# Kernel optimization log

Hardware: AMD Instinct MI355X
Metric: run time of the kernel (lower is better)

The kernel has to match this reference:

```python
import jax, jax.numpy as jnp
import numpy as np

N_NODES = 50000
N_EDGES = 800000
D_IN = 128
D_HID = 128
N_CLASSES = 40


def setup_inputs() -> dict:
    key = jax.random.key(0)
    ks = jax.random.split(key, 12)
    x = jax.random.normal(ks[0], (N_NODES, D_IN), dtype=jnp.float32)
    edge_index = jax.random.randint(ks[1], (2, N_EDGES), 0, N_NODES, dtype=jnp.int64)
    s1 = 1.0 / np.sqrt(D_IN)
    s2 = 1.0 / np.sqrt(D_HID)
    W1 = jax.random.uniform(ks[2], (D_IN, D_HID), jnp.float32, -s1, s1)
    b1 = jnp.zeros((D_HID,), jnp.float32)
    W2 = jax.random.uniform(ks[3], (D_HID, D_HID), jnp.float32, -s2, s2)
    b2 = jnp.zeros((D_HID,), jnp.float32)
    W3 = jax.random.uniform(ks[4], (D_HID, D_HID), jnp.float32, -s2, s2)
    b3 = jnp.zeros((D_HID,), jnp.float32)
    fcW = jax.random.uniform(ks[5], (D_HID, N_CLASSES), jnp.float32, -s2, s2)
    fcb = jax.random.uniform(ks[6], (N_CLASSES,), jnp.float32, -s2, s2)
    return {"x": x, "edge_index": edge_index, "W1": W1, "b1": b1,
            "W2": W2, "b2": b2, "W3": W3, "b3": b3, "fcW": fcW, "fcb": fcb}


def _gcn_norm(edge_index, n_nodes):
    # add self-loops, compute symmetric normalization deg^-1/2[src]*deg^-1/2[dst]
    loops = jnp.arange(n_nodes, dtype=edge_index.dtype)
    src = jnp.concatenate([edge_index[0], loops])
    dst = jnp.concatenate([edge_index[1], loops])
    deg = jax.ops.segment_sum(jnp.ones_like(dst, dtype=jnp.float32), dst,
                              num_segments=n_nodes)
    dinv = jax.lax.rsqrt(deg)  # deg >= 1 thanks to self-loops
    norm = dinv[src] * dinv[dst]  # [E+N]
    return src, dst, norm


def _gcn_conv(h, W, b, src, dst, norm, n_nodes):
    h = h @ W                               # [N, D]
    msg = h[src] * norm[:, None]            # [E+N, D] gather + scale
    out = jax.ops.segment_sum(msg, dst, num_segments=n_nodes)  # scatter-add
    return out + b


def reference(x, edge_index, W1, b1, W2, b2, W3, b3, fcW, fcb):
    n = x.shape[0]
    src, dst, norm = _gcn_norm(edge_index, n)
    h = jax.nn.relu(_gcn_conv(x, W1, b1, src, dst, norm, n))
    h = jax.nn.relu(_gcn_conv(h, W2, b2, src, dst, norm, n))
    h = jax.nn.relu(_gcn_conv(h, W3, b3, src, dst, norm, n))
    out = h @ fcW + fcb
    return (h, out)
```

## Files before the change

### kernel.cpp

```cpp
#include <hip/hip_runtime.h>
#include <hip/hip_fp16.h>

#define NN 50000
#define NE 800000
#define D  128
#define NC 40
#define NBLK ((NN + 255) / 256)
#define NXCD 8
#define DRANGE ((NN + NXCD - 1) / NXCD)
#define EPB 2048
#define NCH ((NE + EPB - 1) / EPB)
#define CAP 64
#define NTILE ((NN + 127) / 128)

typedef short bf16x8 __attribute__((ext_vector_type(8)));
typedef float f32x16 __attribute__((ext_vector_type(16)));

__device__ __forceinline__ void load_edge(const void* ei, int e, int is64, int& s, int& d) {
    if (is64) {
        const long long* p = (const long long*)ei;
        s = (int)p[e]; d = (int)p[NE + e];
    } else {
        const int* p = (const int*)ei;
        s = p[e]; d = p[NE + e];
    }
}

__global__ __launch_bounds__(256) void setup_kernel(int* __restrict__ cnt,
                                                    const int* __restrict__ ei,
                                                    int* __restrict__ flag) {
    if (blockIdx.x == NBLK) {
        __shared__ int nz;
        if (threadIdx.x == 0) nz = 0;
        __syncthreads();
        int c = 0;
        for (int i = threadIdx.x; i < 2048; i += 256)
            if (ei[2 * i + 1] != 0) c = 1;
        if (c) atomicAdd(&nz, 1);
        __syncthreads();
        if (threadIdx.x == 0) *flag = (nz == 0) ? 1 : 0;
    } else {
        int i = blockIdx.x * 256 + threadIdx.x;
        if (i < NN) cnt[i] = 0;
    }
}

__global__ __launch_bounds__(256) void fill_kernel(const void* ei, const int* __restrict__ flag,
                                                   int* cnt, int* __restrict__ srcs) {
    int r = blockIdx.x & (NXCD - 1);
    int chunk = blockIdx.x >> 3;
    int base = chunk * EPB;
    int dlo = r * DRANGE, dhi = dlo + DRANGE;
    int is64 = *flag;
#pragma unroll
    for (int j = 0; j < EPB / 256; ++j) {
        int e = base + threadIdx.x + j * 256;
        if (e >= NE) break;
        int s, d; load_edge(ei, e, is64, s, d);
        if (d < dlo || d >= dhi || (unsigned)d >= NN || (unsigned)s >= NN) continue;
        int slot = atomicAdd(&cnt[d], 1);
        if (slot < CAP) srcs[d * CAP + slot] = s;
    }
}

__global__ __launch_bounds__(256) void sort_kernel(const int* __restrict__ cnt,
                                                   int* __restrict__ srcs,
                                                   float* __restrict__ dinv) {
    int wid = (blockIdx.x * 256 + threadIdx.x) >> 6;
    int lane = threadIdx.x & 63;
    if (wid >= NN) return;
    int deg_raw = cnt[wid];
    if (lane == 0) dinv[wid] = 1.0f / sqrtf((float)deg_raw + 1.0f);
    int deg = (deg_raw > CAP) ? CAP : deg_raw;
    if (deg <= 1) return;
    int base = wid * CAP;
    int v = (lane < deg) ? srcs[base + lane] : 0x7fffffff;
#pragma unroll
    for (int k = 2; k <= 64; k <<= 1) {
#pragma unroll
        for (int j = k >> 1; j > 0; j >>= 1) {
            int o = __shfl_xor(v, j);
            bool up = ((lane & k) == 0);
            bool lower = ((lane & j) == 0);
            int mn = min(v, o), mx = max(v, o);
            v = (lower == up) ? mn : mx;
        }
    }
    if (lane < deg) srcs[base + lane] = v;
}

__device__ __forceinline__ ushort f2bf(float x) {
    unsigned u = __float_as_uint(x);
    return (ushort)((u + 0x7fffu + ((u >> 16) & 1u)) >> 16);
}
__device__ __forceinline__ float bf2f(ushort h) {
    return __uint_as_float(((unsigned)h) << 16);
}

__global__ __launch_bounds__(128) void prep_all_kernel(const float* __restrict__ W1,
                                                       const float* __restrict__ W2,
                                                       const float* __restrict__ W3,
                                                       const float* __restrict__ fcW,
                                                       ushort* __restrict__ i1,
                                                       ushort* __restrict__ i2,
                                                       ushort* __restrict__ i3,
                                                       ushort* __restrict__ ifc) {
    int b = blockIdx.x;
    int k = threadIdx.x;
    if (b < 384) {
        const float* W = (b < 128) ? W1 : (b < 256) ? W2 : W3;
        ushort* img = (b < 128) ? i1 : (b < 256) ? i2 : i3;
        int c = b & 127;
        float w = W[(size_t)k * D + c];
        ushort hi = f2bf(w);
        ushort lo = f2bf(w - bf2f(hi));
        int ch = k >> 6, kk = k & 63, g = kk >> 3;
        int idx = c * 64 + ((g ^ (c & 7)) * 8) + (kk & 7);
        img[(size_t)(ch * 2 + 0) * 8192 + idx] = hi;
        img[(size_t)(ch * 2 + 1) * 8192 + idx] = lo;
    } else {
        int c = b - 384;
        float w = (c < NC) ? fcW[(size_t)k * NC + c] : 0.0f;
        ushort hi = f2bf(w);
        ushort lo = f2bf(w - bf2f(hi));
        int g = k >> 3;
        int idx = c * 128 + ((g ^ (c & 7)) * 8) + (k & 7);
        ifc[idx] = hi;
        ifc[8192 + idx] = lo;
    }
}


__global__ __launch_bounds__(256, 2) void gemm_f32_kernel(const float* __restrict__ A,
                                                          const ushort* __restrict__ Wimg,
                                                          ushort* __restrict__ T) {
    __shared__ alignas(16) ushort sAh[8192];
    __shared__ alignas(16) ushort sAl[8192];
    __shared__ alignas(16) ushort sWh[8192];
    __shared__ alignas(16) ushort sWl[8192];
    int tid = threadIdx.x;
    int wave = tid >> 6, lane = tid & 63;
    int wr = wave >> 1, wc = wave & 1;
    int m0 = blockIdx.x * 128;
    f32x16 acc[2][2];
#pragma unroll
    for (int i = 0; i < 2; ++i)
#pragma unroll
        for (int j = 0; j < 2; ++j)
#pragma unroll
            for (int q = 0; q < 16; ++q) acc[i][j][q] = 0.0f;

    for (int ch = 0; ch < 2; ++ch) {
        const float4* wh = (const float4*)(Wimg + (size_t)(ch * 2 + 0) * 8192);
        const float4* wl = (const float4*)(Wimg + (size_t)(ch * 2 + 1) * 8192);
#pragma unroll
        for (int i = 0; i < 4; ++i) {
            ((float4*)sWh)[tid + i * 256] = wh[tid + i * 256];
            ((float4*)sWl)[tid + i * 256] = wl[tid + i * 256];
        }
#pragma unroll
        for (int p = 0; p < 8; ++p) {
            int idx = tid + p * 256;
            int r = idx >> 4;
            int kq = idx & 15;
            float4 v = make_float4(0, 0, 0, 0);
            int grow = m0 + r;
            if (grow < NN) v = *(const float4*)(A + (size_t)grow * D + ch * 64 + kq * 4);
            ushort4 h, l;
            h.x = f2bf(v.x); l.x = f2bf(v.x - bf2f(h.x));
            h.y = f2bf(v.y); l.y = f2bf(v.y - bf2f(h.y));
            h.z = f2bf(v.z); l.z = f2bf(v.z - bf2f(h.z));
            h.w = f2bf(v.w); l.w = f2bf(v.w - bf2f(h.w));
            int g = kq >> 1, half = kq & 1;
            int uidx = r * 64 + ((g ^ (r & 7)) * 8) + half * 4;
            *(ushort4*)&sAh[uidx] = h;
            *(ushort4*)&sAl[uidx] = l;
        }
        __syncthreads();

        int rb = wr * 64 + (lane & 31);
        int cb = wc * 64 + (lane & 31);
#pragma unroll
        for (int s = 0; s < 4; ++s) {
            int gg = s * 2 + (lane >> 5);
            int ra0 = rb, ra1 = rb + 32;
            int ca0 = cb, ca1 = cb + 32;
            bf16x8 ah0 = *(const bf16x8*)&sAh[ra0 * 64 + ((gg ^ (ra0 & 7)) * 8)];
            bf16x8 ah1 = *(const bf16x8*)&sAh[ra1 * 64 + ((gg ^ (ra1 & 7)) * 8)];
            bf16x8 al0 = *(const bf16x8*)&sAl[ra0 * 64 + ((gg ^ (ra0 & 7)) * 8)];
            bf16x8 al1 = *(const bf16x8*)&sAl[ra1 * 64 + ((gg ^ (ra1 & 7)) * 8)];
            bf16x8 wh0 = *(const bf16x8*)&sWh[ca0 * 64 + ((gg ^ (ca0 & 7)) * 8)];
            bf16x8 wh1 = *(const bf16x8*)&sWh[ca1 * 64 + ((gg ^ (ca1 & 7)) * 8)];
            bf16x8 wl0 = *(const bf16x8*)&sWl[ca0 * 64 + ((gg ^ (ca0 & 7)) * 8)];
            bf16x8 wl1 = *(const bf16x8*)&sWl[ca1 * 64 + ((gg ^ (ca1 & 7)) * 8)];
            acc[0][0] = __builtin_amdgcn_mfma_f32_32x32x16_bf16(ah0, wh0, acc[0][0], 0, 0, 0);
            acc[0][0] = __builtin_amdgcn_mfma_f32_32x32x16_bf16(ah0, wl0, acc[0][0], 0, 0, 0);
            acc[0][0] = __builtin_amdgcn_mfma_f32_32x32x16_bf16(al0, wh0, acc[0][0], 0, 0, 0);
            acc[0][1] = __builtin_amdgcn_mfma_f32_32x32x16_bf16(ah0, wh1, acc[0][1], 0, 0, 0);
            acc[0][1] = __builtin_amdgcn_mfma_f32_32x32x16_bf16(ah0, wl1, acc[0][1], 0, 0, 0);
            acc[0][1] = __builtin_amdgcn_mfma_f32_32x32x16_bf16(al0, wh1, acc[0][1], 0, 0, 0);
            acc[1][0] = __builtin_amdgcn_mfma_f32_32x32x16_bf16(ah1, wh0, acc[1][0], 0, 0, 0);
            acc[1][0] = __builtin_amdgcn_mfma_f32_32x32x16_bf16(ah1, wl0, acc[1][0], 0, 0, 0);
            acc[1][0] = __builtin_amdgcn_mfma_f32_32x32x16_bf16(al1, wh0, acc[1][0], 0, 0, 0);
            acc[1][1] = __builtin_amdgcn_mfma_f32_32x32x16_bf16(ah1, wh1, acc[1][1], 0, 0, 0);
            acc[1][1] = __builtin_amdgcn_mfma_f32_32x32x16_bf16(ah1, wl1, acc[1][1], 0, 0, 0);
            acc[1][1] = __builtin_amdgcn_mfma_f32_32x32x16_bf16(al1, wh1, acc[1][1], 0, 0, 0);
        }
        __syncthreads();
    }
#pragma unroll
    for (int rt = 0; rt < 2; ++rt)
#pragma unroll
        for (int ct = 0; ct < 2; ++ct) {
            int cg = wc * 64 + ct * 32 + (lane & 31);
#pragma unroll
            for (int reg = 0; reg < 16; ++reg) {
                int row = m0 + wr * 64 + rt * 32 + (reg & 3) + 8 * (reg >> 2) + 4 * (lane >> 5);
                if (row < NN)
                    T[(size_t)row * D + cg] = __half_as_ushort(__float2half(acc[rt][ct][reg]));
            }
        }
}

__global__ __launch_bounds__(256, 2) void gemm_img_kernel(const ushort* __restrict__ Aimg,
                                                          const ushort* __restrict__ Wimg,
                                                          ushort* __restrict__ T) {
    __shared__ alignas(16) ushort sAh[8192];
    __shared__ alignas(16) ushort sAl[8192];
    __shared__ alignas(16) ushort sWh[8192];
    __shared__ alignas(16) ushort sWl[8192];
    int tid = threadIdx.x;
    int wave = tid >> 6, lane = tid & 63;
    int wr = wave >> 1, wc = wave & 1;
    int m0 = blockIdx.x * 128;
    const ushort* Atile = Aimg + (size_t)blockIdx.x * 32768;
    f32x16 acc[2][2];
#pragma unroll
    for (int i = 0; i < 2; ++i)
#pragma unroll
        for (int j = 0; j < 2; ++j)
#pragma unroll
            for (int q = 0; q < 16; ++q) acc[i][j][q] = 0.0f;

    for (int ch = 0; ch < 2; ++ch) {
        const float4* wh = (const float4*)(Wimg + (size_t)(ch * 2 + 0) * 8192);
        const float4* wl = (const float4*)(Wimg + (size_t)(ch * 2 + 1) * 8192);
        const float4* ah = (const float4*)(Atile + (size_t)(ch * 2 + 0) * 8192);
        const float4* al = (const float4*)(Atile + (size_t)(ch * 2 + 1) * 8192);
#pragma unroll
        for (int i = 0; i < 4; ++i) {
            ((float4*)sWh)[tid + i * 256] = wh[tid + i * 256];
            ((float4*)sWl)[tid + i * 256] = wl[tid + i * 256];
            ((float4*)sAh)[tid + i * 256] = ah[tid + i * 256];
            ((float4*)sAl)[tid + i * 256] = al[tid + i * 256];
        }
        __syncthreads();

        int rb = wr * 64 + (lane & 31);
        int cb = wc * 64 + (lane & 31);
#pragma unroll
        for (int s = 0; s < 4; ++s) {
            int gg = s * 2 + (lane >> 5);
            int ra0 = rb, ra1 = rb + 32;
            int ca0 = cb, ca1 = cb + 32;
            bf16x8 ah0 = *(const bf16x8*)&sAh[ra0 * 64 + ((gg ^ (ra0 & 7)) * 8)];
            bf16x8 ah1 = *(const bf16x8*)&sAh[ra1 * 64 + ((gg ^ (ra1 & 7)) * 8)];
            bf16x8 al0 = *(const bf16x8*)&sAl[ra0 * 64 + ((gg ^ (ra0 & 7)) * 8)];
            bf16x8 al1 = *(const bf16x8*)&sAl[ra1 * 64 + ((gg ^ (ra1 & 7)) * 8)];
            bf16x8 wh0 = *(const bf16x8*)&sWh[ca0 * 64 + ((gg ^ (ca0 & 7)) * 8)];
            bf16x8 wh1 = *(const bf16x8*)&sWh[ca1 * 64 + ((gg ^ (ca1 & 7)) * 8)];
            bf16x8 wl0 = *(const bf16x8*)&sWl[ca0 * 64 + ((gg ^ (ca0 & 7)) * 8)];
            bf16x8 wl1 = *(const bf16x8*)&sWl[ca1 * 64 + ((gg ^ (ca1 & 7)) * 8)];
            acc[0][0] = __builtin_amdgcn_mfma_f32_32x32x16_bf16(ah0, wh0, acc[0][0], 0, 0, 0);
            acc[0][0] = __builtin_amdgcn_mfma_f32_32x32x16_bf16(ah0, wl0, acc[0][0], 0, 0, 0);
            acc[0][0] = __builtin_amdgcn_mfma_f32_32x32x16_bf16(al0, wh0, acc[0][0], 0, 0, 0);
            acc[0][1] = __builtin_amdgcn_mfma_f32_32x32x16_bf16(ah0, wh1, acc[0][1], 0, 0, 0);
            acc[0][1] = __builtin_amdgcn_mfma_f32_32x32x16_bf16(ah0, wl1, acc[0][1], 0, 0, 0);
            acc[0][1] = __builtin_amdgcn_mfma_f32_32x32x16_bf16(al0, wh1, acc[0][1], 0, 0, 0);
            acc[1][0] = __builtin_amdgcn_mfma_f32_32x32x16_bf16(ah1, wh0, acc[1][0], 0, 0, 0);
            acc[1][0] = __builtin_amdgcn_mfma_f32_32x32x16_bf16(ah1, wl0, acc[1][0], 0, 0, 0);
            acc[1][0] = __builtin_amdgcn_mfma_f32_32x32x16_bf16(al1, wh0, acc[1][0], 0, 0, 0);
            acc[1][1] = __builtin_amdgcn_mfma_f32_32x32x16_bf16(ah1, wh1, acc[1][1], 0, 0, 0);
            acc[1][1] = __builtin_amdgcn_mfma_f32_32x32x16_bf16(ah1, wl1, acc[1][1], 0, 0, 0);
            acc[1][1] = __builtin_amdgcn_mfma_f32_32x32x16_bf16(al1, wh1, acc[1][1], 0, 0, 0);
        }
        __syncthreads();
    }
#pragma unroll
    for (int rt = 0; rt < 2; ++rt)
#pragma unroll
        for (int ct = 0; ct < 2; ++ct) {
            int cg = wc * 64 + ct * 32 + (lane & 31);
#pragma unroll
            for (int reg = 0; reg < 16; ++reg) {
                int row = m0 + wr * 64 + rt * 32 + (reg & 3) + 8 * (reg >> 2) + 4 * (lane >> 5);
                if (row < NN)
                    T[(size_t)row * D + cg] = __half_as_ushort(__float2half(acc[rt][ct][reg]));
            }
        }
}

__global__ __launch_bounds__(256, 2) void fc_mfma_kernel(const float* __restrict__ A,
                                                         const ushort* __restrict__ img,
                                                         const float* __restrict__ b,
                                                         float* __restrict__ O) {
    __shared__ alignas(16) ushort sAh[8192];
    __shared__ alignas(16) ushort sAl[8192];
    __shared__ alignas(16) ushort sWh[8192];
    __shared__ alignas(16) ushort sWl[8192];
    int tid = threadIdx.x;
    int wave = tid >> 6, lane = tid & 63;
    int m0 = blockIdx.x * 128;
#pragma unroll
    for (int i = 0; i < 4; ++i) {
        ((float4*)sWh)[tid + i * 256] = ((const float4*)img)[tid + i * 256];
        ((float4*)sWl)[tid + i * 256] = ((const float4*)(img + 8192))[tid + i * 256];
    }
    f32x16 acc[2];
#pragma unroll
    for (int j = 0; j < 2; ++j)
#pragma unroll
        for (int q = 0; q < 16; ++q) acc[j][q] = 0.0f;

    for (int ch = 0; ch < 2; ++ch) {
#pragma unroll
        for (int p = 0; p < 8; ++p) {
            int idx = tid + p * 256;
            int r = idx >> 4;
            int kq = idx & 15;
            float4 v = make_float4(0, 0, 0, 0);
            int grow = m0 + r;
            if (grow < NN) v = *(const float4*)(A + (size_t)grow * D + ch * 64 + kq * 4);
            ushort4 h, l;
            h.x = f2bf(v.x); l.x = f2bf(v.x - bf2f(h.x));
            h.y = f2bf(v.y); l.y = f2bf(v.y - bf2f(h.y));
            h.z = f2bf(v.z); l.z = f2bf(v.z - bf2f(h.z));
            h.w = f2bf(v.w); l.w = f2bf(v.w - bf2f(h.w));
            int g = kq >> 1, half = kq & 1;
            int uidx = r * 64 + ((g ^ (r & 7)) * 8) + half * 4;
            *(ushort4*)&sAh[uidx] = h;
            *(ushort4*)&sAl[uidx] = l;
        }
        __syncthreads();
        int ra = wave * 32 + (lane & 31);
        int c0 = lane & 31, c1 = 32 + (lane & 31);
#pragma unroll
        for (int s = 0; s < 4; ++s) {
            int gg = s * 2 + (lane >> 5);
            int kg = ch * 8 + gg;
            bf16x8 ah = *(const bf16x8*)&sAh[ra * 64 + ((gg ^ (ra & 7)) * 8)];
            bf16x8 al = *(const bf16x8*)&sAl[ra * 64 + ((gg ^ (ra & 7)) * 8)];
            bf16x8 wh0 = *(const bf16x8*)&sWh[c0 * 128 + ((kg ^ (c0 & 7)) * 8)];
            bf16x8 wl0 = *(const bf16x8*)&sWl[c0 * 128 + ((kg ^ (c0 & 7)) * 8)];
            bf16x8 wh1 = *(const bf16x8*)&sWh[c1 * 128 + ((kg ^ (c1 & 7)) * 8)];
            bf16x8 wl1 = *(const bf16x8*)&sWl[c1 * 128 + ((kg ^ (c1 & 7)) * 8)];
            acc[0] = __builtin_amdgcn_mfma_f32_32x32x16_bf16(ah, wh0, acc[0], 0, 0, 0);
            acc[0] = __builtin_amdgcn_mfma_f32_32x32x16_bf16(ah, wl0, acc[0], 0, 0, 0);
            acc[0] = __builtin_amdgcn_mfma_f32_32x32x16_bf16(al, wh0, acc[0], 0, 0, 0);
            acc[1] = __builtin_amdgcn_mfma_f32_32x32x16_bf16(ah, wh1, acc[1], 0, 0, 0);
            acc[1] = __builtin_amdgcn_mfma_f32_32x32x16_bf16(ah, wl1, acc[1], 0, 0, 0);
            acc[1] = __builtin_amdgcn_mfma_f32_32x32x16_bf16(al, wh1, acc[1], 0, 0, 0);
        }
        __syncthreads();
    }
#pragma unroll
    for (int ct = 0; ct < 2; ++ct) {
        int col = ct * 32 + (lane & 31);
        if (col < NC) {
            float bb = b[col];
#pragma unroll
            for (int reg = 0; reg < 16; ++reg) {
                int row = m0 + wave * 32 + (reg & 3) + 8 * (reg >> 2) + 4 * (lane >> 5);
                if (row < NN) O[(size_t)row * NC + col] = acc[ct][reg] + bb;
            }
        }
    }
}

__device__ __forceinline__ float4 h4load(const ushort* __restrict__ T, int row, int l) {
    uint2 hv = ((const uint2*)(T + (size_t)row * D))[l];
    __half2 h0 = *(__half2*)&hv.x, h1 = *(__half2*)&hv.y;
    float2 f0 = __half22float2(h0), f1 = __half22float2(h1);
    return make_float4(f0.x, f0.y, f1.x, f1.y);
}

template<int IMG>
__global__ __launch_bounds__(256) void aggregate_kernel(const ushort* __restrict__ T,
                                                        const int* __restrict__ cnt,
                                                        const int* __restrict__ srcs,
                                                        const float* __restrict__ dinv,
                                                        const float* __restrict__ b,
                                                        float* __restrict__ out,
                                                        ushort* __restrict__ img) {
    int wid = (blockIdx.x * 256 + threadIdx.x) >> 6;
    int lane = threadIdx.x & 63;
    int h = lane >> 5, l = lane & 31;
    if (wid >= NN) return;
    float di = dinv[wid];
    float wself = h ? 0.0f : di * di;
    float4 acc = h4load(T, wid, l);
    acc.x *= wself; acc.y *= wself; acc.z *= wself; acc.w *= wself;
    int beg = wid * CAP;
    int deg = cnt[wid]; if (deg > CAP) deg = CAP;
    int end = beg + deg;
    int e = beg;
    for (; e + 7 < end; e += 8) {
        int s0 = srcs[e + h], s1 = srcs[e + 2 + h];
        int s2 = srcs[e + 4 + h], s3 = srcs[e + 6 + h];
        float w0 = dinv[s0] * di, w1 = dinv[s1] * di;
        float w2 = dinv[s2] * di, w3 = dinv[s3] * di;
        float4 v0 = h4load(T, s0, l);
        float4 v1 = h4load(T, s1, l);
        float4 v2 = h4load(T, s2, l);
        float4 v3 = h4load(T, s3, l);
        acc.x = fmaf(v0.x, w0, acc.x); acc.y = fmaf(v0.y, w0, acc.y);
        acc.z = fmaf(v0.z, w0, acc.z); acc.w = fmaf(v0.w, w0, acc.w);
        acc.x = fmaf(v1.x, w1, acc.x); acc.y = fmaf(v1.y, w1, acc.y);
        acc.z = fmaf(v1.z, w1, acc.z); acc.w = fmaf(v1.w, w1, acc.w);
        acc.x = fmaf(v2.x, w2, acc.x); acc.y = fmaf(v2.y, w2, acc.y);
        acc.z = fmaf(v2.z, w2, acc.z); acc.w = fmaf(v2.w, w2, acc.w);
        acc.x = fmaf(v3.x, w3, acc.x); acc.y = fmaf(v3.y, w3, acc.y);
        acc.z = fmaf(v3.z, w3, acc.z); acc.w = fmaf(v3.w, w3, acc.w);
    }
    for (; e + 1 < end; e += 2) {
        int s0 = srcs[e + h];
        float w0 = dinv[s0] * di;
        float4 v0 = h4load(T, s0, l);
        acc.x = fmaf(v0.x, w0, acc.x); acc.y = fmaf(v0.y, w0, acc.y);
        acc.z = fmaf(v0.z, w0, acc.z); acc.w = fmaf(v0.w, w0, acc.w);
    }
    if (e < end) {
        int ee = (e + h < end) ? e + h : end - 1;
        int s0 = srcs[ee];
        float w0 = (e + h < end) ? dinv[s0] * di : 0.0f;
        float4 v0 = h4load(T, s0, l);
        acc.x = fmaf(v0.x, w0, acc.x); acc.y = fmaf(v0.y, w0, acc.y);
        acc.z = fmaf(v0.z, w0, acc.z); acc.w = fmaf(v0.w, w0, acc.w);
    }
    acc.x += __shfl_xor(acc.x, 32);
    acc.y += __shfl_xor(acc.y, 32);
    acc.z += __shfl_xor(acc.z, 32);
    acc.w += __shfl_xor(acc.w, 32);
    if (h == 0) {
        float4 bb = ((const float4*)b)[l];
        acc.x = fmaxf(acc.x + bb.x, 0.0f);
        acc.y = fmaxf(acc.y + bb.y, 0.0f);
        acc.z = fmaxf(acc.z + bb.z, 0.0f);
        acc.w = fmaxf(acc.w + bb.w, 0.0f);
        if (IMG) {
            int tile = wid >> 7, rr = wid & 127;
            int c0 = 4 * l;
            int ch = c0 >> 6, kk = c0 & 63, g = kk >> 3;
            int idx = rr * 64 + ((g ^ (rr & 7)) * 8) + (kk & 7);
            ushort4 hh, ll;
            hh.x = f2bf(acc.x); ll.x = f2bf(acc.x - bf2f(hh.x));
            hh.y = f2bf(acc.y); ll.y = f2bf(acc.y - bf2f(hh.y));
            hh.z = f2bf(acc.z); ll.z = f2bf(acc.z - bf2f(hh.z));
            hh.w = f2bf(acc.w); ll.w = f2bf(acc.w - bf2f(hh.w));
            ushort* base = img + (size_t)tile * 32768;
            *(ushort4*)(base + (size_t)(ch * 2 + 0) * 8192 + idx) = hh;
            *(ushort4*)(base + (size_t)(ch * 2 + 1) * 8192 + idx) = ll;
        } else {
            ((float4*)(out + (size_t)wid * D))[l] = acc;
        }
    }
}

extern "C" void kernel_launch(void* const* d_in, const int* in_sizes, int n_in,
                              void* d_out, int out_size, void* d_ws, size_t ws_size,
                              hipStream_t stream) {
    const float* x   = (const float*)d_in[0];
    const void*  ei  = d_in[1];
    const float* W1  = (const float*)d_in[2];
    const float* b1  = (const float*)d_in[3];
    const float* W2  = (const float*)d_in[4];
    const float* b2  = (const float*)d_in[5];
    const float* W3  = (const float*)d_in[6];
    const float* b3  = (const float*)d_in[7];
    const float* fcW = (const float*)d_in[8];
    const float* fcb = (const float*)d_in[9];

    float* out_h  = (float*)d_out;
    float* out_fc = out_h + (size_t)NN * D;

    size_t off = 0;
    auto alloc = [&](size_t bytes) {
        void* p = (char*)d_ws + off;
        off += (bytes + 255) & ~(size_t)255;
        return p;
    };
    float*  dinv   = (float*) alloc((size_t)NN * 4);
    int*    cnt    = (int*)   alloc((size_t)NN * 4);
    int*    flag   = (int*)   alloc(256);
    int*    srcs   = (int*)   alloc((size_t)NN * CAP * 4);
    ushort* bufT   = (ushort*)alloc((size_t)NN * D * 2);
    ushort* himg   = (ushort*)alloc((size_t)NTILE * 32768 * 2);
    ushort* wimg1  = (ushort*)alloc(32768 * 2);
    ushort* wimg2  = (ushort*)alloc(32768 * 2);
    ushort* wimg3  = (ushort*)alloc(32768 * 2);
    ushort* fcimg  = (ushort*)alloc(16384 * 2);
    (void)ws_size; (void)in_sizes; (void)n_in; (void)out_size;

    setup_kernel<<<NBLK + 1, 256, 0, stream>>>(cnt, (const int*)ei, flag);
    prep_all_kernel<<<448, 128, 0, stream>>>(W1, W2, W3, fcW, wimg1, wimg2, wimg3, fcimg);
    fill_kernel<<<NCH * NXCD, 256, 0, stream>>>(ei, flag, cnt, srcs);
    sort_kernel<<<(NN * 64 + 255) / 256, 256, 0, stream>>>(cnt, srcs, dinv);

    int agg_grid = (NN * 64 + 255) / 256;
    gemm_f32_kernel<<<NTILE, 256, 0, stream>>>(x, wimg1, bufT);
    aggregate_kernel<1><<<agg_grid, 256, 0, stream>>>(bufT, cnt, srcs, dinv, b1, nullptr, himg);
    gemm_img_kernel<<<NTILE, 256, 0, stream>>>(himg, wimg2, bufT);
    aggregate_kernel<1><<<agg_grid, 256, 0, stream>>>(bufT, cnt, srcs, dinv, b2, nullptr, himg);
    gemm_img_kernel<<<NTILE, 256, 0, stream>>>(himg, wimg3, bufT);
    aggregate_kernel<0><<<agg_grid, 256, 0, stream>>>(bufT, cnt, srcs, dinv, b3, out_h, nullptr);

    fc_mfma_kernel<<<NTILE, 256, 0, stream>>>(out_h, fcimg, fcb, out_fc);
}
```

Before: 232.1 us.

## Precompute per-edge normalization weights and use one half-wave per node in aggregation

A separate kernel now computes dinv first. The sort kernel then writes a per-edge weight array (dinv[src]*dinv[dst]) next to the sorted source lists, so each aggregation pass no longer performs a dependent dinv gather per edge. The aggregation kernel also changes from one 64-lane wave per node, split into two halves over edges, to one 32-lane group per node with an 8-way unrolled gather, which removes the cross-half shuffle reduction and doubles the nodes per block. The cost is an extra launch plus an NN*CAP float buffer that must be written once and read three times, and fewer memory loads in flight per node.

```diff
diff --git a/kernel.cpp b/kernel.cpp
--- a/kernel.cpp
+++ b/kernel.cpp
@@ -63,16 +63,22 @@
     }
 }
 
+__global__ __launch_bounds__(256) void dinv_kernel(const int* __restrict__ cnt,
+                                                   float* __restrict__ dinv) {
+    int i = blockIdx.x * 256 + threadIdx.x;
+    if (i < NN) dinv[i] = 1.0f / sqrtf((float)cnt[i] + 1.0f);
+}
+
 __global__ __launch_bounds__(256) void sort_kernel(const int* __restrict__ cnt,
                                                    int* __restrict__ srcs,
-                                                   float* __restrict__ dinv) {
+                                                   float* __restrict__ wts,
+                                                   const float* __restrict__ dinv) {
     int wid = (blockIdx.x * 256 + threadIdx.x) >> 6;
     int lane = threadIdx.x & 63;
     if (wid >= NN) return;
-    int deg_raw = cnt[wid];
-    if (lane == 0) dinv[wid] = 1.0f / sqrtf((float)deg_raw + 1.0f);
-    int deg = (deg_raw > CAP) ? CAP : deg_raw;
-    if (deg <= 1) return;
+    int deg = cnt[wid]; if (deg > CAP) deg = CAP;
+    if (deg == 0) return;
+    float di = dinv[wid];
     int base = wid * CAP;
     int v = (lane < deg) ? srcs[base + lane] : 0x7fffffff;
 #pragma unroll
@@ -86,7 +92,10 @@
             v = (lower == up) ? mn : mx;
         }
     }
-    if (lane < deg) srcs[base + lane] = v;
+    if (lane < deg) {
+        srcs[base + lane] = v;
+        wts[base + lane] = dinv[v] * di;
+    }
 }
 
 __device__ __forceinline__ ushort f2bf(float x) {
@@ -130,7 +139,6 @@
     }
 }
 
-
 __global__ __launch_bounds__(256, 2) void gemm_f32_kernel(const float* __restrict__ A,
                                                           const ushort* __restrict__ Wimg,
                                                           ushort* __restrict__ T) {
@@ -384,85 +392,75 @@
     return make_float4(f0.x, f0.y, f1.x, f1.y);
 }
 
+__device__ __forceinline__ void fma4(float4& a, float4 v, float w) {
+    a.x = fmaf(v.x, w, a.x); a.y = fmaf(v.y, w, a.y);
+    a.z = fmaf(v.z, w, a.z); a.w = fmaf(v.w, w, a.w);
+}
+
 template<int IMG>
 __global__ __launch_bounds__(256) void aggregate_kernel(const ushort* __restrict__ T,
                                                         const int* __restrict__ cnt,
                                                         const int* __restrict__ srcs,
+                                                        const float* __restrict__ wts,
                                                         const float* __restrict__ dinv,
                                                         const float* __restrict__ b,
                                                         float* __restrict__ out,
                                                         ushort* __restrict__ img) {
-    int wid = (blockIdx.x * 256 + threadIdx.x) >> 6;
-    int lane = threadIdx.x & 63;
-    int h = lane >> 5, l = lane & 31;
+    int wid = (blockIdx.x * 256 + threadIdx.x) >> 5;
+    int l = threadIdx.x & 31;
     if (wid >= NN) return;
     float di = dinv[wid];
-    float wself = h ? 0.0f : di * di;
+    float wself = di * di;
     float4 acc = h4load(T, wid, l);
     acc.x *= wself; acc.y *= wself; acc.z *= wself; acc.w *= wself;
-    int beg = wid * CAP;
+    int base = wid * CAP;
     int deg = cnt[wid]; if (deg > CAP) deg = CAP;
-    int end = beg + deg;
-    int e = beg;
-    for (; e + 7 < end; e += 8) {
-        int s0 = srcs[e + h], s1 = srcs[e + 2 + h];
-        int s2 = srcs[e + 4 + h], s3 = srcs[e + 6 + h];
-        float w0 = dinv[s0] * di, w1 = dinv[s1] * di;
-        float w2 = dinv[s2] * di, w3 = dinv[s3] * di;
-        float4 v0 = h4load(T, s0, l);
-        float4 v1 = h4load(T, s1, l);
-        float4 v2 = h4load(T, s2, l);
-        float4 v3 = h4load(T, s3, l);
-        acc.x = fmaf(v0.x, w0, acc.x); acc.y = fmaf(v0.y, w0, acc.y);
-        acc.z = fmaf(v0.z, w0, acc.z); acc.w = fmaf(v0.w, w0, acc.w);
-        acc.x = fmaf(v1.x, w1, acc.x); acc.y = fmaf(v1.y, w1, acc.y);
-        acc.z = fmaf(v1.z, w1, acc.z); acc.w = fmaf(v1.w, w1, acc.w);
-        acc.x = fmaf(v2.x, w2, acc.x); acc.y = fmaf(v2.y, w2, acc.y);
-        acc.z = fmaf(v2.z, w2, acc.z); acc.w = fmaf(v2.w, w2, acc.w);
-        acc.x = fmaf(v3.x, w3, acc.x); acc.y = fmaf(v3.y, w3, acc.y);
-        acc.z = fmaf(v3.z, w3, acc.z); acc.w = fmaf(v3.w, w3, acc.w);
-    }
-    for (; e + 1 < end; e += 2) {
-        int s0 = srcs[e + h];
-        float w0 = dinv[s0] * di;
-        float4 v0 = h4load(T, s0, l);
-        acc.x = fmaf(v0.x, w0, acc.x); acc.y = fmaf(v0.y, w0, acc.y);
-        acc.z = fmaf(v0.z, w0, acc.z); acc.w = fmaf(v0.w, w0, acc.w);
-    }
-    if (e < end) {
-        int ee = (e + h < end) ? e + h : end - 1;
-        int s0 = srcs[ee];
-        float w0 = (e + h < end) ? dinv[s0] * di : 0.0f;
-        float4 v0 = h4load(T, s0, l);
-        acc.x = fmaf(v0.x, w0, acc.x); acc.y = fmaf(v0.y, w0, acc.y);
-        acc.z = fmaf(v0.z, w0, acc.z); acc.w = fmaf(v0.w, w0, acc.w);
-    }
-    acc.x += __shfl_xor(acc.x, 32);
-    acc.y += __shfl_xor(acc.y, 32);
-    acc.z += __shfl_xor(acc.z, 32);
-    acc.w += __shfl_xor(acc.w, 32);
-    if (h == 0) {
-        float4 bb = ((const float4*)b)[l];
-        acc.x = fmaxf(acc.x + bb.x, 0.0f);
-        acc.y = fmaxf(acc.y + bb.y, 0.0f);
-        acc.z = fmaxf(acc.z + bb.z, 0.0f);
-        acc.w = fmaxf(acc.w + bb.w, 0.0f);
-        if (IMG) {
-            int tile = wid >> 7, rr = wid & 127;
-            int c0 = 4 * l;
-            int ch = c0 >> 6, kk = c0 & 63, g = kk >> 3;
-            int idx = rr * 64 + ((g ^ (rr & 7)) * 8) + (kk & 7);
-            ushort4 hh, ll;
-            hh.x = f2bf(acc.x); ll.x = f2bf(acc.x - bf2f(hh.x));
-            hh.y = f2bf(acc.y); ll.y = f2bf(acc.y - bf2f(hh.y));
-            hh.z = f2bf(acc.z); ll.z = f2bf(acc.z - bf2f(hh.z));
-            hh.w = f2bf(acc.w); ll.w = f2bf(acc.w - bf2f(hh.w));
-            ushort* base = img + (size_t)tile * 32768;
-            *(ushort4*)(base + (size_t)(ch * 2 + 0) * 8192 + idx) = hh;
-            *(ushort4*)(base + (size_t)(ch * 2 + 1) * 8192 + idx) = ll;
-        } else {
-            ((float4*)(out + (size_t)wid * D))[l] = acc;
-        }
+    int e = 0;
+    for (; e + 7 < deg; e += 8) {
+        int s0 = srcs[base + e + 0], s1 = srcs[base + e + 1];
+        int s2 = srcs[base + e + 2], s3 = srcs[base + e + 3];
+        int s4 = srcs[base + e + 4], s5 = srcs[base + e + 5];
+        int s6 = srcs[base + e + 6], s7 = srcs[base + e + 7];
+        float4 v0 = h4load(T, s0, l), v1 = h4load(T, s1, l);
+        float4 v2 = h4load(T, s2, l), v3 = h4load(T, s3, l);
+        float4 v4 = h4load(T, s4, l), v5 = h4load(T, s5, l);
+        float4 v6 = h4load(T, s6, l), v7 = h4load(T, s7, l);
+        fma4(acc, v0, wts[base + e + 0]); fma4(acc, v1, wts[base + e + 1]);
+        fma4(acc, v2, wts[base + e + 2]); fma4(acc, v3, wts[base + e + 3]);
+        fma4(acc, v4, wts[base + e + 4]); fma4(acc, v5, wts[base + e + 5]);
+        fma4(acc, v6, wts[base + e + 6]); fma4(acc, v7, wts[base + e + 7]);
+    }
+    for (; e + 3 < deg; e += 4) {
+        int s0 = srcs[base + e + 0], s1 = srcs[base + e + 1];
+        int s2 = srcs[base + e + 2], s3 = srcs[base + e + 3];
+        float4 v0 = h4load(T, s0, l), v1 = h4load(T, s1, l);
+        float4 v2 = h4load(T, s2, l), v3 = h4load(T, s3, l);
+        fma4(acc, v0, wts[base + e + 0]); fma4(acc, v1, wts[base + e + 1]);
+        fma4(acc, v2, wts[base + e + 2]); fma4(acc, v3, wts[base + e + 3]);
+    }
+    for (; e < deg; ++e) {
+        fma4(acc, h4load(T, srcs[base + e], l), wts[base + e]);
+    }
+    float4 bb = ((const float4*)b)[l];
+    acc.x = fmaxf(acc.x + bb.x, 0.0f);
+    acc.y = fmaxf(acc.y + bb.y, 0.0f);
+    acc.z = fmaxf(acc.z + bb.z, 0.0f);
+    acc.w = fmaxf(acc.w + bb.w, 0.0f);
+    if (IMG) {
+        int tile = wid >> 7, rr = wid & 127;
+        int c0 = 4 * l;
+        int ch = c0 >> 6, kk = c0 & 63, g = kk >> 3;
+        int idx = rr * 64 + ((g ^ (rr & 7)) * 8) + (kk & 7);
+        ushort4 hh, ll;
+        hh.x = f2bf(acc.x); ll.x = f2bf(acc.x - bf2f(hh.x));
+        hh.y = f2bf(acc.y); ll.y = f2bf(acc.y - bf2f(hh.y));
+        hh.z = f2bf(acc.z); ll.z = f2bf(acc.z - bf2f(hh.z));
+        hh.w = f2bf(acc.w); ll.w = f2bf(acc.w - bf2f(hh.w));
+        ushort* bimg = img + (size_t)tile * 32768;
+        *(ushort4*)(bimg + (size_t)(ch * 2 + 0) * 8192 + idx) = hh;
+        *(ushort4*)(bimg + (size_t)(ch * 2 + 1) * 8192 + idx) = ll;
+    } else {
+        ((float4*)(out + (size_t)wid * D))[l] = acc;
     }
 }
 
@@ -493,6 +491,7 @@
     int*    cnt    = (int*)   alloc((size_t)NN * 4);
     int*    flag   = (int*)   alloc(256);
     int*    srcs   = (int*)   alloc((size_t)NN * CAP * 4);
+    float*  wts    = (float*) alloc((size_t)NN * CAP * 4);
     ushort* bufT   = (ushort*)alloc((size_t)NN * D * 2);
     ushort* himg   = (ushort*)alloc((size_t)NTILE * 32768 * 2);
     ushort* wimg1  = (ushort*)alloc(32768 * 2);
@@ -504,15 +503,16 @@
     setup_kernel<<<NBLK + 1, 256, 0, stream>>>(cnt, (const int*)ei, flag);
     prep_all_kernel<<<448, 128, 0, stream>>>(W1, W2, W3, fcW, wimg1, wimg2, wimg3, fcimg);
     fill_kernel<<<NCH * NXCD, 256, 0, stream>>>(ei, flag, cnt, srcs);
-    sort_kernel<<<(NN * 64 + 255) / 256, 256, 0, stream>>>(cnt, srcs, dinv);
-
-    int agg_grid = (NN * 64 + 255) / 256;
+    dinv_kernel<<<NBLK, 256, 0, stream>>>(cnt, dinv);
+    sort_kernel<<<(NN * 64 + 255) / 256, 256, 0, stream>>>(cnt, srcs, wts, dinv);
+
+    int agg_grid = (NN * 32 + 255) / 256;
     gemm_f32_kernel<<<NTILE, 256, 0, stream>>>(x, wimg1, bufT);
-    aggregate_kernel<1><<<agg_grid, 256, 0, stream>>>(bufT, cnt, srcs, dinv, b1, nullptr, himg);
+    aggregate_kernel<1><<<agg_grid, 256, 0, stream>>>(bufT, cnt, srcs, wts, dinv, b1, nullptr, himg);
     gemm_img_kernel<<<NTILE, 256, 0, stream>>>(himg, wimg2, bufT);
-    aggregate_kernel<1><<<agg_grid, 256, 0, stream>>>(bufT, cnt, srcs, dinv, b2, nullptr, himg);
+    aggregate_kernel<1><<<agg_grid, 256, 0, stream>>>(bufT, cnt, srcs, wts, dinv, b2, nullptr, himg);
     gemm_img_kernel<<<NTILE, 256, 0, stream>>>(himg, wimg3, bufT);
-    aggregate_kernel<0><<<agg_grid, 256, 0, stream>>>(bufT, cnt, srcs, dinv, b3, out_h, nullptr);
+    aggregate_kernel<0><<<agg_grid, 256, 0, stream>>>(bufT, cnt, srcs, wts, dinv, b3, out_h, nullptr);
 
     fc_mfma_kernel<<<NTILE, 256, 0, stream>>>(out_h, fcimg, fcb, out_fc);
 }
```

Result: faster. 219.9 us (-5.2%).
